# Kernel tuning notes

Hardware: AMD Instinct MI355X
Metric: run time of the kernel (lower is better)

## Reference

```python
import jax, jax.numpy as jnp
import numpy as np
from itertools import combinations
from collections import deque

JOINTS = ['Ab','Chest','Head','Hip','LFArm','LFoot','LHand','LShin','LShoulder','LThigh','LToe','LUArm','Neck','RFArm','RFoot','RHand','RShin','RShoulder','RThigh','RToe','RUArm']
PARENTS = {'Ab':'Hip','Chest':'Ab','Head':'Neck','Hip':'Hip','LFArm':'LUArm','LFoot':'LShin','LHand':'LFArm','LShin':'LThigh','LShoulder':'Chest','LThigh':'Hip','LToe':'LFoot','LUArm':'LShoulder','Neck':'Chest','RFArm':'RUArm','RFoot':'RShin','RHand':'RFArm','RShin':'RThigh','RShoulder':'Chest','RThigh':'Hip','RToe':'RFoot','RUArm':'RShoulder'}
_idx = {n: i for i, n in enumerate(JOINTS)}
PAR = {_idx[k]: _idx[v] for k, v in PARENTS.items()}
NJ = 21
_adj = {j: [] for j in range(NJ)}
for j, p in PAR.items():
    if j != p:
        _adj[j].append(p); _adj[p].append(j)

def _bfs_path(u, v):
    # unique shortest path in the kinematic tree == nx.all_pairs_shortest_path
    prev = {u: None}; q = deque([u])
    while q:
        x = q.popleft()
        if x == v:
            break
        for y in _adj[x]:
            if y not in prev:
                prev[y] = x; q.append(y)
    path = [v]
    while prev[path[-1]] is not None:
        path.append(prev[path[-1]])
    return path[::-1]

PAIRS = list(combinations(range(NJ), 2))  # 210 pairs
# Precompute signed path-sum matrix C (input side) and endpoint-diff matrix T (target side)
C_np = np.zeros((len(PAIRS), NJ), np.float32)
T_np = np.zeros((len(PAIRS), NJ), np.float32)
for pi, (u, v) in enumerate(PAIRS):
    pa = _bfs_path(u, v)
    for m in range(len(pa) - 1):
        C_np[pi, pa[m]] += 1.0 if PAR[pa[m]] == pa[m + 1] else -1.0
    T_np[pi, u] += 1.0; T_np[pi, v] -= 1.0
C = jnp.asarray(C_np)
T = jnp.asarray(T_np)


def setup_inputs() -> dict:
    key = jax.random.key(0)
    k1, k2 = jax.random.split(key)
    B = 65536
    return {
        'input': jax.random.normal(k1, (B, NJ * 3), jnp.float32),
        'target': jax.random.normal(k2, (B, NJ * 3), jnp.float32),
    }


def reference(input, target):
    B = input.shape[0]
    bi = input.reshape(B, NJ, 3)   # bone vectors
    bt = target.reshape(B, NJ, 3)
    # [B, 210, 3]: signed path sum of predicted bones minus gt endpoint difference
    delta = jnp.einsum('pj,bjc->bpc', C, bi) - jnp.einsum('pj,bjc->bpc', T, bt)
    norms = jnp.abs(delta).sum(-1)          # per-sample L1 norm per pair [B, 210]
    return norms.mean(0).sum().reshape(1)   # mean over batch, summed over pairs
```

## Files before the change

### kernel.cpp

```cpp
#include <hip/hip_runtime.h>

#define NJ 21
#define NPAIR 210
#define TPB 128
#define ROWF 63

constexpr int PAR_[NJ] = {3,0,12,3,11,7,4,9,1,3,5,8,1,20,16,13,18,1,3,14,17};

constexpr int depth_of(int x){ int d=0; while(PAR_[x]!=x){ x=PAR_[x]; ++d; } return d; }
constexpr int lca_of(int u,int v){
  int du=depth_of(u), dv=depth_of(v);
  while(du>dv){ u=PAR_[u]; --du; }
  while(dv>du){ v=PAR_[v]; --dv; }
  while(u!=v){ u=PAR_[u]; v=PAR_[v]; }
  return u;
}

struct PairTab { unsigned char u[NPAIR], v[NPAIR], L[NPAIR]; };
constexpr PairTab make_pairs(){
  PairTab t{};
  int k=0;
  for(int u=0;u<NJ;++u) for(int v=u+1;v<NJ;++v){
    t.u[k]=(unsigned char)u; t.v[k]=(unsigned char)v;
    t.L[k]=(unsigned char)lca_of(u,v); ++k;
  }
  return t;
}
constexpr PairTab PT = make_pairs();

constexpr int TOPO_[NJ] = {3,0,1,12,2,8,11,4,6,17,20,13,15,9,7,5,10,18,16,14,19};
constexpr int PV_[NJ]   = {3,0,12,21,11,7,4,9,1,3,5,8,1,20,16,13,18,1,3,14,17};

__global__ __launch_bounds__(TPB, 1)
void comp_loss_kernel(const float* __restrict__ in, const float* __restrict__ tg,
                      float* __restrict__ out, float invB)
{
  __shared__ float sIn[TPB*ROWF];
  __shared__ float sTg[TPB*ROWF];
  const int tid = threadIdx.x;
  const long long blockBase = (long long)blockIdx.x * (TPB*ROWF);

  {
    const float4* gi = (const float4*)(in + blockBase);
    const float4* gt = (const float4*)(tg + blockBase);
    float4* si = (float4*)sIn;
    float4* st = (float4*)sTg;
    constexpr int N4 = TPB*ROWF/4;
    for (int i = tid; i < N4; i += TPB){ si[i]=gi[i]; st[i]=gt[i]; }
  }
  __syncthreads();

  float bn[ROWF], tt[ROWF];
  {
    const float* r  = sIn + tid*ROWF;
    const float* r2 = sTg + tid*ROWF;
    #pragma unroll
    for(int k=0;k<ROWF;++k) bn[k]=r[k];
    #pragma unroll
    for(int k=0;k<ROWF;++k) tt[k]=r2[k];
  }

  float A[66];
  #pragma unroll
  for(int c=0;c<3;++c) A[63+c] = 0.f;
  #pragma unroll
  for(int i=0;i<NJ;++i){
    constexpr auto T = TOPO_;
    const int j = T[i];
    const int p = PAR_[j];
    #pragma unroll
    for(int c=0;c<3;++c)
      A[j*3+c] = (j==3) ? bn[j*3+c] : (bn[j*3+c] + A[p*3+c]);
  }

  float F[ROWF], G[ROWF];
  #pragma unroll
  for(int j=0;j<NJ;++j){
    const int p = PV_[j];
    #pragma unroll
    for(int c=0;c<3;++c){
      F[j*3+c] = A[j*3+c] - tt[j*3+c];
      G[j*3+c] = A[p*3+c] - tt[j*3+c];
    }
  }

  float acc = 0.f;
  #pragma unroll
  for(int p=0;p<NPAIR;++p){
    const int u = PT.u[p], v = PT.v[p], L = PT.L[p];
    #pragma unroll
    for(int c=0;c<3;++c){
      const float d = F[u*3+c] - G[v*3+c] - bn[L*3+c];
      acc += fabsf(d);
    }
  }

  #pragma unroll
  for(int off=32; off>0; off>>=1) acc += __shfl_down(acc, off, 64);
  __syncthreads();
  if ((tid & 63) == 0) sIn[tid>>6] = acc;
  __syncthreads();
  if (tid == 0){
    float bs = 0.f;
    #pragma unroll
    for(int w=0; w<TPB/64; ++w) bs += sIn[w];
    atomicAdd(out, bs * invB);
  }
}

extern "C" void kernel_launch(void* const* d_in, const int* in_sizes, int n_in,
                              void* d_out, int out_size, void* d_ws, size_t ws_size,
                              hipStream_t stream) {
  const float* in = (const float*)d_in[0];
  const float* tg = (const float*)d_in[1];
  float* out = (float*)d_out;
  const int B = in_sizes[0] / (NJ*3);
  hipMemsetAsync(out, 0, out_size * sizeof(float), stream);
  const int grid = B / TPB;
  comp_loss_kernel<<<grid, TPB, 0, stream>>>(in, tg, out, 1.0f/(float)B);
}
```

Before: 84.78 us.

## Split each sample's xyz components across three threads to cut register pressure

Each sample is now processed by three threads, one per coordinate axis, so per-thread arrays shrink from 63 to 21 floats. Blocks hold 64 samples with 192 threads, and launch bounds raise the occupancy hint. The pair loop uses three independent accumulators, and G is derived from F minus the bone. This trades more threads and strided shared-memory reads for much lower register usage and better latency hiding.

```diff
diff --git a/kernel.cpp b/kernel.cpp
--- a/kernel.cpp
+++ b/kernel.cpp
@@ -2,10 +2,12 @@
 
 #define NJ 21
 #define NPAIR 210
-#define TPB 128
+#define SPB 64
+#define TPB 192
 #define ROWF 63
 
 constexpr int PAR_[NJ] = {3,0,12,3,11,7,4,9,1,3,5,8,1,20,16,13,18,1,3,14,17};
+constexpr int TOPO_[NJ] = {3,0,1,12,2,8,11,4,6,17,20,13,15,9,7,5,10,18,16,14,19};
 
 constexpr int depth_of(int x){ int d=0; while(PAR_[x]!=x){ x=PAR_[x]; ++d; } return d; }
 constexpr int lca_of(int u,int v){
@@ -28,72 +30,58 @@
 }
 constexpr PairTab PT = make_pairs();
 
-constexpr int TOPO_[NJ] = {3,0,1,12,2,8,11,4,6,17,20,13,15,9,7,5,10,18,16,14,19};
-constexpr int PV_[NJ]   = {3,0,12,21,11,7,4,9,1,3,5,8,1,20,16,13,18,1,3,14,17};
-
-__global__ __launch_bounds__(TPB, 1)
+__global__ __launch_bounds__(TPB, 4)
 void comp_loss_kernel(const float* __restrict__ in, const float* __restrict__ tg,
                       float* __restrict__ out, float invB)
 {
-  __shared__ float sIn[TPB*ROWF];
-  __shared__ float sTg[TPB*ROWF];
+  __shared__ float sIn[SPB*ROWF];
+  __shared__ float sTg[SPB*ROWF];
   const int tid = threadIdx.x;
-  const long long blockBase = (long long)blockIdx.x * (TPB*ROWF);
+  const long long blockBase = (long long)blockIdx.x * (SPB*ROWF);
 
   {
     const float4* gi = (const float4*)(in + blockBase);
     const float4* gt = (const float4*)(tg + blockBase);
     float4* si = (float4*)sIn;
     float4* st = (float4*)sTg;
-    constexpr int N4 = TPB*ROWF/4;
+    constexpr int N4 = SPB*ROWF/4;
     for (int i = tid; i < N4; i += TPB){ si[i]=gi[i]; st[i]=gt[i]; }
   }
   __syncthreads();
 
-  float bn[ROWF], tt[ROWF];
-  {
-    const float* r  = sIn + tid*ROWF;
-    const float* r2 = sTg + tid*ROWF;
-    #pragma unroll
-    for(int k=0;k<ROWF;++k) bn[k]=r[k];
-    #pragma unroll
-    for(int k=0;k<ROWF;++k) tt[k]=r2[k];
+  const int s = tid / 3;
+  const int c = tid - 3*s;
+  const float* rI = sIn + s*ROWF + c;
+  const float* rT = sTg + s*ROWF + c;
+
+  float bn[NJ];
+  #pragma unroll
+  for(int j=0;j<NJ;++j) bn[j] = rI[3*j];
+
+  float A[NJ];
+  #pragma unroll
+  for(int i=0;i<NJ;++i){
+    const int j = TOPO_[i];
+    const int p = PAR_[j];
+    A[j] = (j==3) ? bn[j] : (bn[j] + A[p]);
   }
 
-  float A[66];
+  float F[NJ], G[NJ];
   #pragma unroll
-  for(int c=0;c<3;++c) A[63+c] = 0.f;
-  #pragma unroll
-  for(int i=0;i<NJ;++i){
-    constexpr auto T = TOPO_;
-    const int j = T[i];
-    const int p = PAR_[j];
-    #pragma unroll
-    for(int c=0;c<3;++c)
-      A[j*3+c] = (j==3) ? bn[j*3+c] : (bn[j*3+c] + A[p*3+c]);
+  for(int j=0;j<NJ;++j){
+    const float t = rT[3*j];
+    F[j] = A[j] - t;
+    G[j] = F[j] - bn[j];
   }
 
-  float F[ROWF], G[ROWF];
+  float a0=0.f, a1=0.f, a2=0.f;
   #pragma unroll
-  for(int j=0;j<NJ;++j){
-    const int p = PV_[j];
-    #pragma unroll
-    for(int c=0;c<3;++c){
-      F[j*3+c] = A[j*3+c] - tt[j*3+c];
-      G[j*3+c] = A[p*3+c] - tt[j*3+c];
-    }
+  for(int p=0;p<NPAIR;p+=3){
+    a0 += fabsf(F[PT.u[p  ]] - G[PT.v[p  ]] - bn[PT.L[p  ]]);
+    a1 += fabsf(F[PT.u[p+1]] - G[PT.v[p+1]] - bn[PT.L[p+1]]);
+    a2 += fabsf(F[PT.u[p+2]] - G[PT.v[p+2]] - bn[PT.L[p+2]]);
   }
-
-  float acc = 0.f;
-  #pragma unroll
-  for(int p=0;p<NPAIR;++p){
-    const int u = PT.u[p], v = PT.v[p], L = PT.L[p];
-    #pragma unroll
-    for(int c=0;c<3;++c){
-      const float d = F[u*3+c] - G[v*3+c] - bn[L*3+c];
-      acc += fabsf(d);
-    }
-  }
+  float acc = (a0 + a1) + a2;
 
   #pragma unroll
   for(int off=32; off>0; off>>=1) acc += __shfl_down(acc, off, 64);
@@ -116,6 +104,6 @@
   float* out = (float*)d_out;
   const int B = in_sizes[0] / (NJ*3);
   hipMemsetAsync(out, 0, out_size * sizeof(float), stream);
-  const int grid = B / TPB;
+  const int grid = B / SPB;
   comp_loss_kernel<<<grid, TPB, 0, stream>>>(in, tg, out, 1.0f/(float)B);
 }
```

Measured after the change: 88.33 us. 4.2% more time.
